# Kernel tuning notes

Measured on AMD Instinct MI355X. Metric: run time of the kernel, lower is better.

## Reference

```python
import jax, jax.numpy as jnp
import numpy as np
from jax import lax

B, C, H, W = 4, 512, 32, 32
HEADS, HC, GROUPS = 8, 64, 4
GC = C // GROUPS          # group channels = 128
GH = HEADS // GROUPS      # heads per group = 2
KK = 5                    # offset conv kernel (stage_idx=2)
OFFSET_RANGE_FACTOR = 2.0
LN_EPS = 1e-5


def conv1x1(x, w, b):
    # x: [B,Cin,H,W], w: [Cout,Cin], b: [Cout]
    return jnp.einsum('bchw,oc->bohw', x, w) + b[None, :, None, None]


def ref_points(h, w, n, dtype=jnp.float32):
    # torch linspace(0.5, h-0.5, h) normalized to (-1,1); stacked (y,x)
    ry = ((jnp.arange(h, dtype=dtype) + 0.5) / h) * 2.0 - 1.0
    rx = ((jnp.arange(w, dtype=dtype) + 0.5) / w) * 2.0 - 1.0
    ref = jnp.stack(jnp.meshgrid(ry, rx, indexing='ij'), axis=-1)  # [h,w,2]
    return jnp.broadcast_to(ref[None], (n, h, w, 2))


def grid_sample(img, grid):
    # F.grid_sample: bilinear, align_corners=True, padding_mode='zeros'
    # img: [N,C,Hs,Ws], grid: [N,*S,2] with grid[...,0]=x, grid[...,1]=y in [-1,1]
    N, Cc, Hs, Ws = img.shape
    gx = (grid[..., 0] + 1.0) * 0.5 * (Ws - 1)
    gy = (grid[..., 1] + 1.0) * 0.5 * (Hs - 1)
    x0 = jnp.floor(gx)
    y0 = jnp.floor(gy)
    wx1 = gx - x0
    wy1 = gy - y0
    imgf = img.reshape(N, Cc, Hs * Ws)

    def corner(ix, iy, wgt):
        valid = ((ix >= 0) & (ix <= Ws - 1) & (iy >= 0) & (iy <= Hs - 1)).astype(img.dtype)
        flat = (jnp.clip(iy, 0, Hs - 1) * Ws + jnp.clip(ix, 0, Ws - 1)).astype(jnp.int32)
        vals = jax.vmap(lambda im, f: im[:, f])(imgf, flat)  # [N,C,*S]
        return vals * (wgt * valid)[:, None]

    return (corner(x0, y0, (1 - wx1) * (1 - wy1))
            + corner(x0 + 1, y0, wx1 * (1 - wy1))
            + corner(x0, y0 + 1, (1 - wx1) * wy1)
            + corner(x0 + 1, y0 + 1, wx1 * wy1))


def setup_inputs() -> dict:
    key = jax.random.key(0)
    ks = jax.random.split(key, 10)

    def w(k, shape, s=0.02):
        return jax.random.normal(k, shape, jnp.float32) * s

    return {
        'x': jax.random.normal(ks[0], (B, C, H, W), jnp.float32),
        'w_q': w(ks[1], (C, C)), 'b_q': jnp.zeros((C,), jnp.float32),
        'w_k': w(ks[2], (C, C)), 'b_k': jnp.zeros((C,), jnp.float32),
        'w_v': w(ks[3], (C, C)), 'b_v': jnp.zeros((C,), jnp.float32),
        'w_o': w(ks[4], (C, C)), 'b_o': jnp.zeros((C,), jnp.float32),
        'dw_w': w(ks[5], (GC, 1, KK, KK), 0.05),  # depthwise offset conv
        'dw_b': jnp.zeros((GC,), jnp.float32),
        'ln_g': jnp.ones((GC,), jnp.float32),
        'ln_b': jnp.zeros((GC,), jnp.float32),
        'off_w': w(ks[6], (2, GC), 0.05),          # 1x1 conv -> 2 offset channels
        'rpe': w(ks[7], (HEADS, 2 * H - 1, 2 * W - 1), 0.01),
    }


def reference(x, w_q, b_q, w_k, b_k, w_v, b_v, w_o, b_o,
              dw_w, dw_b, ln_g, ln_b, off_w, rpe):
    q = conv1x1(x, w_q, b_q)
    # 'b (g c) h w -> (b g) c h w'
    q_off = q.reshape(B * GROUPS, GC, H, W)
    # depthwise conv kk=5, stride=1, pad=2
    off = lax.conv_general_dilated(q_off, dw_w, (1, 1),
                                   ((KK // 2, KK // 2), (KK // 2, KK // 2)),
                                   dimension_numbers=('NCHW', 'OIHW', 'NCHW'),
                                   feature_group_count=GC) + dw_b[None, :, None, None]
    # LayerNormProxy over channel dim
    mu = jnp.mean(off, axis=1, keepdims=True)
    var = jnp.mean((off - mu) ** 2, axis=1, keepdims=True)
    off = (off - mu) * lax.rsqrt(var + LN_EPS) * ln_g[None, :, None, None] + ln_b[None, :, None, None]
    off = jax.nn.gelu(off, approximate=False)
    off = jnp.einsum('bchw,oc->bohw', off, off_w)  # [B*G, 2, Hk, Wk] (y,x channels)
    Hk, Wk = off.shape[2], off.shape[3]
    nS = Hk * Wk
    off_range = jnp.array([1.0 / Hk, 1.0 / Wk], dtype=x.dtype).reshape(1, 2, 1, 1)
    off = jnp.tanh(off) * off_range * OFFSET_RANGE_FACTOR
    off = jnp.transpose(off, (0, 2, 3, 1))  # [B*G, Hk, Wk, 2]
    ref = ref_points(Hk, Wk, B * GROUPS, x.dtype)
    pos = off + ref  # offset_range_factor >= 0 branch
    # deformable sampling (grid takes (x,y))
    xs = grid_sample(x.reshape(B * GROUPS, GC, H, W), pos[..., ::-1])  # [B*G,GC,Hk,Wk]
    xs = xs.reshape(B, C, 1, nS)
    qf = q.reshape(B * HEADS, HC, H * W)
    k = conv1x1(xs, w_k, b_k).reshape(B * HEADS, HC, nS)
    v = conv1x1(xs, w_v, b_v).reshape(B * HEADS, HC, nS)
    attn = jnp.einsum('bcm,bcn->bmn', qf, k) * (HC ** -0.5)  # [B*Hd, HW, nS]
    # continuous relative-position bias via bilinear table lookup
    rpe_b = jnp.broadcast_to(rpe[None], (B,) + rpe.shape).reshape(
        B * GROUPS, GH, rpe.shape[1], rpe.shape[2])
    q_grid = ref_points(H, W, B * GROUPS, x.dtype)
    disp = (q_grid.reshape(B * GROUPS, H * W, 1, 2)
            - pos.reshape(B * GROUPS, 1, nS, 2)) * 0.5  # [B*G, HW, nS, 2]
    bias = grid_sample(rpe_b, disp[..., ::-1]).reshape(B * HEADS, H * W, nS)
    attn = jax.nn.softmax(attn + bias, axis=2)
    out = jnp.einsum('bmn,bcn->bcm', attn, v).reshape(B, C, H, W)
    y = conv1x1(out, w_o, b_o)
    return (y,
            pos.reshape(B, GROUPS, Hk, Wk, 2),
            ref.reshape(B, GROUPS, Hk, Wk, 2))
```

## Files before the change

### kernel.cpp

```cpp
#include <hip/hip_runtime.h>
#include <hip/hip_bf16.h>

typedef __hip_bfloat16 bf16;
typedef __attribute__((ext_vector_type(8))) short bf16x8;
typedef __attribute__((ext_vector_type(4))) float f32x4;

#define BDIM 4
#define CDIM 512
#define NHEADS 8
#define NGROUPS 4
#define GCH 128

__device__ __forceinline__ float bf2f(bf16 v) { return __bfloat162float(v); }
__device__ __forceinline__ float bfu2f(unsigned short u) {
  return __uint_as_float(((unsigned)u) << 16);
}
__device__ __forceinline__ unsigned short f2bu(float v) {
  return __hip_bfloat16_raw(__float2bfloat16(v)).x;
}
__device__ __forceinline__ unsigned pack2(float lo, float hi) {
  return (unsigned)f2bu(lo) | ((unsigned)f2bu(hi) << 16);
}

__global__ __launch_bounds__(256) void cvt_kernel(
    const float* __restrict__ x, const float* __restrict__ wq,
    const float* __restrict__ wk, const float* __restrict__ wv,
    const float* __restrict__ wo, unsigned short* __restrict__ x_bf,
    unsigned short* __restrict__ w_bf) {
  const int seg = blockIdx.y;
  const float* src;
  unsigned short* dst;
  int count;
  if (seg == 0) { src = x; dst = x_bf; count = 2097152; }
  else {
    src = (seg == 1 ? wq : seg == 2 ? wk : seg == 3 ? wv : wo);
    dst = w_bf + (seg - 1) * 262144;
    count = 262144;
  }
  const int i = (blockIdx.x * 256 + threadIdx.x) * 8;
  if (i >= count) return;
  const float4 a = *(const float4*)(src + i);
  const float4 b = *(const float4*)(src + i + 4);
  uint4 u;
  u.x = pack2(a.x, a.y);
  u.y = pack2(a.z, a.w);
  u.z = pack2(b.x, b.y);
  u.w = pack2(b.z, b.w);
  *(uint4*)(dst + i) = u;
}

template <typename OutT>
__global__ __launch_bounds__(256) void gemm_kernel(
    const unsigned short* __restrict__ Wb,
    const float* __restrict__ bias,
    const unsigned short* __restrict__ in,
    OutT* __restrict__ out) {
  __shared__ __align__(16) unsigned char smem[16384];
  unsigned char* a_lds = smem;
  unsigned char* b_lds = smem + 8192;
  const int b = blockIdx.z;
  const int o0 = blockIdx.y * 64;
  const int n0 = blockIdx.x * 64;
  const int t = threadIdx.x, l = t & 63, w = t >> 6;
  const int rg = l >> 4, cl = l & 15;
  const int o_base = (w >> 1) * 32, n_base = (w & 1) * 32;
  const unsigned short* inb = in + (size_t)b * 524288;
  const int ao = t >> 2;
  const int ac8 = (t & 3) * 8;
  const int kc2 = (t & 31) * 2;
  const int kn8 = (t >> 5) * 8;

  f32x4 acc[2][2] = {{{0.f,0.f,0.f,0.f},{0.f,0.f,0.f,0.f}},
                     {{0.f,0.f,0.f,0.f},{0.f,0.f,0.f,0.f}}};

  for (int k0 = 0; k0 < 512; k0 += 64) {
    {
      const uint4 wa = *(const uint4*)(Wb + (size_t)(o0 + ao) * 512 + k0 + ac8);
      const uint4 wb2 = *(const uint4*)(Wb + (size_t)(o0 + ao) * 512 + k0 + ac8 + 32);
      const unsigned swo = (unsigned)((ao & 7) << 4);
      *(uint4*)(a_lds + ao * 128 + ((2 * ac8) ^ swo)) = wa;
      *(uint4*)(a_lds + ao * 128 + ((2 * ac8 + 64) ^ swo)) = wb2;
    }
    {
      union { uint4 v; unsigned short hw[8]; } r0, r1;
      r0.v = *(const uint4*)(inb + (size_t)(k0 + kc2) * 1024 + n0 + kn8);
      r1.v = *(const uint4*)(inb + (size_t)(k0 + kc2 + 1) * 1024 + n0 + kn8);
#pragma unroll
      for (int i = 0; i < 8; i++) {
        const int n = kn8 + i;
        const unsigned v32 = (unsigned)r0.hw[i] | ((unsigned)r1.hw[i] << 16);
        *(unsigned*)(b_lds + n * 128 + ((2 * kc2) ^ ((n & 7) << 4))) = v32;
      }
    }
    __syncthreads();
#pragma unroll
    for (int kk = 0; kk < 2; kk++) {
      bf16x8 af[2], bfr[2];
#pragma unroll
      for (int m = 0; m < 2; m++) {
        const int o_loc = o_base + 16 * m + cl;
        af[m] = *(const bf16x8*)(a_lds + o_loc * 128 +
                                 ((64 * kk + 16 * rg) ^ ((o_loc & 7) << 4)));
      }
#pragma unroll
      for (int nn = 0; nn < 2; nn++) {
        const int n_loc = n_base + 16 * nn + cl;
        bfr[nn] = *(const bf16x8*)(b_lds + n_loc * 128 +
                                   ((64 * kk + 16 * rg) ^ ((n_loc & 7) << 4)));
      }
#pragma unroll
      for (int m = 0; m < 2; m++)
#pragma unroll
        for (int nn = 0; nn < 2; nn++)
          acc[m][nn] = __builtin_amdgcn_mfma_f32_16x16x32_bf16(af[m], bfr[nn],
                                                               acc[m][nn], 0, 0, 0);
    }
    __syncthreads();
  }

  float* o_st = (float*)smem;
#pragma unroll
  for (int m = 0; m < 2; m++)
#pragma unroll
    for (int nn = 0; nn < 2; nn++)
#pragma unroll
      for (int r = 0; r < 4; r++)
        o_st[(o_base + 16 * m + 4 * rg + r) * 64 + n_base + 16 * nn + cl] =
            acc[m][nn][r];
  __syncthreads();
  const int eo = t >> 4;
  const int en = (t & 15) * 4;
#pragma unroll
  for (int pass = 0; pass < 4; pass++) {
    const int o_loc = eo + pass * 16;
    const f32x4 v = *(const f32x4*)(o_st + o_loc * 64 + en);
    const float bv = bias[o0 + o_loc];
    if constexpr (sizeof(OutT) == 2) {
      ushort4 u;
      u.x = f2bu(v[0] + bv);
      u.y = f2bu(v[1] + bv);
      u.z = f2bu(v[2] + bv);
      u.w = f2bu(v[3] + bv);
      *(ushort4*)((bf16*)out + ((size_t)b * 512 + o0 + o_loc) * 1024 + n0 + en) = u;
    } else {
      float4 r = {v[0] + bv, v[1] + bv, v[2] + bv, v[3] + bv};
      *(float4*)((float*)out + ((size_t)b * 512 + o0 + o_loc) * 1024 + n0 + en) = r;
    }
  }
}

__global__ __launch_bounds__(512) void offset_kernel(
    const bf16* __restrict__ q, const float* __restrict__ dw_w,
    const float* __restrict__ dw_b, const float* __restrict__ ln_g,
    const float* __restrict__ ln_b, const float* __restrict__ off_w,
    float* __restrict__ pos, float* __restrict__ out_pos, float* __restrict__ out_ref) {
  __shared__ unsigned short q_s[5][36][128];
  __shared__ float red_a[4][2][2];
  __shared__ float red_p[4][2][2];
  const int bg = blockIdx.x;
  const int h = blockIdx.y;
  const int b = bg >> 2, g = bg & 3;
  const int t = threadIdx.x;

  for (int task = t; task < 640; task += 512) {
    const int ky = task >> 7, c = task & 127;
    const int y = h + ky - 2;
    if (y >= 0 && y < 32) {
      const unsigned short* qrow =
          (const unsigned short*)q + ((size_t)b * CDIM + g * GCH + c) * 1024 + y * 32;
      q_s[ky][0][c] = 0;
      q_s[ky][1][c] = 0;
#pragma unroll
      for (int x8 = 0; x8 < 4; x8++) {
        union { uint4 u; unsigned short s[8]; } vv;
        vv.u = *(const uint4*)(qrow + x8 * 8);
#pragma unroll
        for (int i = 0; i < 8; i++) q_s[ky][2 + x8 * 8 + i][c] = vv.s[i];
      }
      q_s[ky][34][c] = 0;
      q_s[ky][35][c] = 0;
    } else {
#pragma unroll
      for (int xi = 0; xi < 36; xi++) q_s[ky][xi][c] = 0;
    }
  }

  const int wslot = t >> 7;
  const int c = t & 127;
  const int half = c >> 6;
  const int lane = t & 63;
  float wgt[25];
#pragma unroll
  for (int i = 0; i < 25; i++) wgt[i] = dw_w[c * 25 + i];
  const float cbias = dw_b[c];
  const float gam = ln_g[c], bet = ln_b[c];
  const float ow0 = off_w[c], ow1 = off_w[GCH + c];
  __syncthreads();

  for (int j = 0; j < 8; j++) {
    const int w = wslot * 8 + j;
    float s = cbias;
#pragma unroll
    for (int ky = 0; ky < 5; ky++)
#pragma unroll
      for (int kx = 0; kx < 5; kx++)
        s += wgt[ky * 5 + kx] * bfu2f(q_s[ky][w + kx][c]);
    float ssum = s, ssq = s * s;
#pragma unroll
    for (int o = 1; o < 64; o <<= 1) {
      ssum += __shfl_xor(ssum, o);
      ssq += __shfl_xor(ssq, o);
    }
    if (lane == 0) { red_a[wslot][half][0] = ssum; red_a[wslot][half][1] = ssq; }
    __syncthreads();
    const float mu = (red_a[wslot][0][0] + red_a[wslot][1][0]) * (1.0f / 128.0f);
    const float var = (red_a[wslot][0][1] + red_a[wslot][1][1]) * (1.0f / 128.0f) - mu * mu;
    const float xn = (s - mu) * rsqrtf(var + 1e-5f) * gam + bet;
    const float ge = 0.5f * xn * (1.0f + erff(xn * 0.70710678118654752f));
    float p0 = ow0 * ge, p1 = ow1 * ge;
#pragma unroll
    for (int o = 1; o < 64; o <<= 1) {
      p0 += __shfl_xor(p0, o);
      p1 += __shfl_xor(p1, o);
    }
    if (lane == 0) { red_p[wslot][half][0] = p0; red_p[wslot][half][1] = p1; }
    __syncthreads();
    if (c == 0) {
      const float oy = tanhf(red_p[wslot][0][0] + red_p[wslot][1][0]) * 0.0625f;
      const float ox = tanhf(red_p[wslot][0][1] + red_p[wslot][1][1]) * 0.0625f;
      const float ry = ((float)h + 0.5f) * (2.0f / 32.0f) - 1.0f;
      const float rx = ((float)w + 0.5f) * (2.0f / 32.0f) - 1.0f;
      const float py = oy + ry, px = ox + rx;
      const size_t idx = (size_t)bg * 1024 + h * 32 + w;
      pos[idx * 2] = py;
      pos[idx * 2 + 1] = px;
      out_pos[idx * 2] = py;
      out_pos[idx * 2 + 1] = px;
      out_ref[idx * 2] = ry;
      out_ref[idx * 2 + 1] = rx;
    }
  }
}

__global__ __launch_bounds__(256) void sample_kernel(
    const float* __restrict__ x, const float* __restrict__ pos, bf16* __restrict__ xs) {
  const int bg = blockIdx.x, c = blockIdx.y;
  const int b = bg >> 2, g = bg & 3;
  __shared__ float plane[1024];
  const float* xp = x + ((size_t)b * CDIM + g * GCH + c) * 1024;
  for (int i = threadIdx.x; i < 1024; i += 256) plane[i] = xp[i];
  __syncthreads();
  for (int s = threadIdx.x; s < 1024; s += 256) {
    const float py = pos[((size_t)bg * 1024 + s) * 2];
    const float px = pos[((size_t)bg * 1024 + s) * 2 + 1];
    const float gx = (px + 1.0f) * 15.5f;
    const float gy = (py + 1.0f) * 15.5f;
    const float x0f = floorf(gx), y0f = floorf(gy);
    const float wx = gx - x0f, wy = gy - y0f;
    const int ix = (int)x0f, iy = (int)y0f;
    float r = 0.0f;
    const bool vx0 = (ix >= 0) & (ix <= 31), vx1 = (ix + 1 >= 0) & (ix + 1 <= 31);
    const bool vy0 = (iy >= 0) & (iy <= 31), vy1 = (iy + 1 >= 0) & (iy + 1 <= 31);
    if (vy0 && vx0) r += plane[iy * 32 + ix] * (1.0f - wx) * (1.0f - wy);
    if (vy0 && vx1) r += plane[iy * 32 + ix + 1] * wx * (1.0f - wy);
    if (vy1 && vx0) r += plane[(iy + 1) * 32 + ix] * (1.0f - wx) * wy;
    if (vy1 && vx1) r += plane[(iy + 1) * 32 + ix + 1] * wx * wy;
    xs[((size_t)bg * GCH + c) * 1024 + s] = __float2bfloat16(r);
  }
}

__global__ __launch_bounds__(512) void attn_kernel(
    const bf16* __restrict__ q, const bf16* __restrict__ kk,
    const bf16* __restrict__ vv, const float* __restrict__ pos,
    const float* __restrict__ rpe, bf16* __restrict__ ao) {
  __shared__ __align__(16) unsigned char smem[68384];
  float* rpe_f = (float*)(smem + 49152);
  float* m_x = (float*)(smem + 67360);
  float* s_x = (float*)(smem + 67872);

  const int bh = blockIdx.y;
  const int m0 = blockIdx.x * 64;
  const int b = bh >> 3, h = bh & 7;
  const int g = h >> 1;
  const int bg = b * 4 + g;
  const int t = threadIdx.x, l = t & 63, w = t >> 6;
  const int wq = w & 3, half = w >> 2;
  const int rg = l >> 4, cl = l & 15;
  const int t2 = t & 255;
  const size_t hbase = ((size_t)b * CDIM + h * 64) * 1024;
  const unsigned short* qu = (const unsigned short*)q;

  unsigned char* k_base = smem + half * 8192;
  unsigned char* v_base = smem + 16384 + half * 8192;
  unsigned char* p_base = smem + 32768 + half * 8192;
  float* pos_a = (float*)(smem + 66336) + half * 128;

  for (int i = t; i < 65 * 66; i += 512) {
    const int y = i / 66, x = i - y * 66;
    float v = 0.0f;
    if (y >= 1 && y <= 63 && x >= 1 && x <= 63)
      v = rpe[h * 3969 + (y - 1) * 63 + (x - 1)];
    rpe_f[i] = v;
  }

  const int qloc = 16 * wq + cl;
  const int qm = m0 + qloc;
  const float qy15 = 15.5f * (((float)(qm >> 5) + 0.5f) * (2.0f / 32.0f) - 1.0f);
  const float qx15 = 15.5f * (((float)(qm & 31) + 0.5f) * (2.0f / 32.0f) - 1.0f);

  bf16x8 bq[2];
#pragma unroll
  for (int kc = 0; kc < 2; kc++) {
    bf16x8 a;
#pragma unroll
    for (int j = 0; j < 8; j++)
      a[j] = (short)qu[hbase + (size_t)(32 * kc + 8 * rg + j) * 1024 + qm];
    bq[kc] = a;
  }

  float rmax = -1e30f, rsum = 0.0f;
  f32x4 oacc[4] = {{0.f,0.f,0.f,0.f},{0.f,0.f,0.f,0.f},
                   {0.f,0.f,0.f,0.f},{0.f,0.f,0.f,0.f}};

  const float* posb = pos + (size_t)bg * 2048;
  const unsigned swl = (unsigned)((cl & 7) << 4);
  const int kc2 = (t2 & 31) * 2;
  const int kn8 = (t2 >> 5) * 8;
  const int vc = t2 >> 2;
  const int vh = (t2 & 3) * 32;

  for (int tile = 0; tile < 8; tile++) {
    const int n0 = half * 512 + tile * 64;
    {
      union { uint4 v; unsigned short hw[8]; } r0, r1;
      r0.v = *(const uint4*)(kk + hbase + (size_t)kc2 * 1024 + n0 + kn8);
      r1.v = *(const uint4*)(kk + hbase + (size_t)(kc2 + 1) * 1024 + n0 + kn8);
#pragma unroll
      for (int i = 0; i < 8; i++) {
        const int n = kn8 + i;
        const unsigned v32 = (unsigned)r0.hw[i] | ((unsigned)r1.hw[i] << 16);
        *(unsigned*)(k_base + n * 128 + ((kc2 * 2) ^ ((n & 7) << 4))) = v32;
      }
      const uint4 s0 = *(const uint4*)(vv + hbase + (size_t)vc * 1024 + n0 + vh / 2);
      const uint4 s1 = *(const uint4*)(vv + hbase + (size_t)vc * 1024 + n0 + vh / 2 + 8);
      *(uint4*)(v_base + vc * 128 + (vh ^ ((vc & 7) << 4))) = s0;
      *(uint4*)(v_base + vc * 128 + ((vh + 16) ^ ((vc & 7) << 4))) = s1;
      if (t2 < 128) pos_a[t2] = 31.0f - 15.5f * posb[2 * n0 + t2];
    }
    __syncthreads();

    f32x4 sf[4];
#pragma unroll
    for (int tn = 0; tn < 4; tn++) {
      const int nrow = 16 * tn + cl;
      const bf16x8 a0 = *(const bf16x8*)(k_base + nrow * 128 + ((16 * rg) ^ swl));
      const bf16x8 a1 = *(const bf16x8*)(k_base + nrow * 128 + ((64 + 16 * rg) ^ swl));
      f32x4 z = {0.f, 0.f, 0.f, 0.f};
      z = __builtin_amdgcn_mfma_f32_16x16x32_bf16(a0, bq[0], z, 0, 0, 0);
      z = __builtin_amdgcn_mfma_f32_16x16x32_bf16(a1, bq[1], z, 0, 0, 0);
      sf[tn] = z;
    }

#pragma unroll
    for (int tn = 0; tn < 4; tn++)
#pragma unroll
      for (int r = 0; r < 4; r++) {
        const int key = 16 * tn + 4 * rg + r;
        const float gyc = qy15 + pos_a[2 * key];
        const float gxc = qx15 + pos_a[2 * key + 1];
        const float y0f = floorf(gyc), x0f = floorf(gxc);
        const float wy = gyc - y0f, wx = gxc - x0f;
        const int iy1 = (int)y0f + 1, ix1 = (int)x0f + 1;
        const float* tp = rpe_f + iy1 * 66 + ix1;
        const float t00 = tp[0], t01 = tp[1];
        const float t10 = tp[66], t11 = tp[67];
        const float r0v = t00 + (t01 - t00) * wx;
        const float r1v = t10 + (t11 - t10) * wx;
        const float bias = r0v + (r1v - r0v) * wy;
        sf[tn][r] = sf[tn][r] * 0.125f + bias;
      }

    float tmax = sf[0][0];
#pragma unroll
    for (int tn = 0; tn < 4; tn++)
#pragma unroll
      for (int r = 0; r < 4; r++) tmax = fmaxf(tmax, sf[tn][r]);
    tmax = fmaxf(tmax, __shfl_xor(tmax, 16));
    tmax = fmaxf(tmax, __shfl_xor(tmax, 32));
    const float nmax = fmaxf(rmax, tmax);
    const float corr = __expf(rmax - nmax);
    rmax = nmax;
    float lsum = 0.0f;
    unsigned pw[8];
#pragma unroll
    for (int tn = 0; tn < 4; tn++) {
      const float p0 = __expf(sf[tn][0] - nmax);
      const float p1 = __expf(sf[tn][1] - nmax);
      const float p2 = __expf(sf[tn][2] - nmax);
      const float p3 = __expf(sf[tn][3] - nmax);
      lsum += (p0 + p1) + (p2 + p3);
      pw[2 * tn] = pack2(p0, p1);
      pw[2 * tn + 1] = pack2(p2, p3);
    }
    lsum += __shfl_xor(lsum, 16);
    lsum += __shfl_xor(lsum, 32);
    rsum = rsum * corr + lsum;
#pragma unroll
    for (int tc = 0; tc < 4; tc++) {
      oacc[tc][0] *= corr; oacc[tc][1] *= corr;
      oacc[tc][2] *= corr; oacc[tc][3] *= corr;
    }

#pragma unroll
    for (int tn = 0; tn < 4; tn++) {
      *(unsigned*)(p_base + qloc * 128 + ((2 * (16 * tn + 4 * rg)) ^ swl)) = pw[2 * tn];
      *(unsigned*)(p_base + qloc * 128 + ((2 * (16 * tn + 4 * rg) + 4) ^ swl)) = pw[2 * tn + 1];
    }

#pragma unroll
    for (int kc = 0; kc < 2; kc++) {
      const bf16x8 pb = *(const bf16x8*)(p_base + qloc * 128 + ((2 * (32 * kc + 8 * rg)) ^ swl));
#pragma unroll
      for (int tc = 0; tc < 4; tc++) {
        const int crow = 16 * tc + cl;
        const bf16x8 av = *(const bf16x8*)(v_base + crow * 128 + ((2 * (32 * kc + 8 * rg)) ^ swl));
        oacc[tc] = __builtin_amdgcn_mfma_f32_16x16x32_bf16(av, pb, oacc[tc], 0, 0, 0);
      }
    }
    __syncthreads();
  }

  if (l < 16) {
    m_x[half * 64 + wq * 16 + cl] = rmax;
    s_x[half * 64 + wq * 16 + cl] = rsum;
  }
  __syncthreads();
  const float m0v = m_x[wq * 16 + cl], m1v = m_x[64 + wq * 16 + cl];
  const float s0v = s_x[wq * 16 + cl], s1v = s_x[64 + wq * 16 + cl];
  const float M = fmaxf(m0v, m1v);
  const float f0 = __expf(m0v - M), f1 = __expf(m1v - M);
  const float inv = 1.0f / (f0 * s0v + f1 * s1v);
  const float scale = (half == 0 ? f0 : f1) * inv;
  float* o_st = (float*)smem;
  if (half == 0) {
#pragma unroll
    for (int tc = 0; tc < 4; tc++)
#pragma unroll
      for (int r = 0; r < 4; r++)
        o_st[(16 * tc + 4 * rg + r) * 66 + qloc] = oacc[tc][r] * scale;
  }
  __syncthreads();
  if (half == 1) {
#pragma unroll
    for (int tc = 0; tc < 4; tc++)
#pragma unroll
      for (int r = 0; r < 4; r++)
        o_st[(16 * tc + 4 * rg + r) * 66 + qloc] += oacc[tc][r] * scale;
  }
  __syncthreads();
  {
    const int c = t >> 3, mq = (t & 7) * 8;
    unsigned u[4];
#pragma unroll
    for (int i = 0; i < 4; i++)
      u[i] = pack2(o_st[c * 66 + mq + 2 * i], o_st[c * 66 + mq + 2 * i + 1]);
    uint4 outv = {u[0], u[1], u[2], u[3]};
    *(uint4*)(ao + hbase + (size_t)c * 1024 + m0 + mq) = outv;
  }
}

extern "C" void kernel_launch(void* const* d_in, const int* in_sizes, int n_in,
                              void* d_out, int out_size, void* d_ws, size_t ws_size,
                              hipStream_t stream) {
  const float* x    = (const float*)d_in[0];
  const float* w_q  = (const float*)d_in[1];
  const float* b_q  = (const float*)d_in[2];
  const float* w_k  = (const float*)d_in[3];
  const float* b_k  = (const float*)d_in[4];
  const float* w_v  = (const float*)d_in[5];
  const float* b_v  = (const float*)d_in[6];
  const float* w_o  = (const float*)d_in[7];
  const float* b_o  = (const float*)d_in[8];
  const float* dw_w = (const float*)d_in[9];
  const float* dw_b = (const float*)d_in[10];
  const float* ln_g = (const float*)d_in[11];
  const float* ln_b = (const float*)d_in[12];
  const float* off_w= (const float*)d_in[13];
  const float* rpe  = (const float*)d_in[14];

  float* out_y   = (float*)d_out;
  float* out_pos = out_y + 2097152;
  float* out_ref = out_pos + 32768;

  float* pos_ws = (float*)d_ws;
  bf16*  q_ws   = (bf16*)(pos_ws + 32768);
  bf16*  xs_ws  = q_ws + 2097152;
  bf16*  k_ws   = xs_ws + 2097152;
  bf16*  v_ws   = k_ws + 2097152;
  bf16*  w_bf   = v_ws + 2097152;
  bf16*  x_bf   = k_ws;
  bf16*  ao_ws  = xs_ws;

  unsigned short* w_bfu = (unsigned short*)w_bf;

  cvt_kernel<<<dim3(1024, 5), 256, 0, stream>>>(x, w_q, w_k, w_v, w_o,
                                                (unsigned short*)x_bf, w_bfu);
  gemm_kernel<bf16><<<dim3(16, 8, 4), 256, 0, stream>>>(
      w_bfu, b_q, (const unsigned short*)x_bf, q_ws);
  offset_kernel<<<dim3(16, 32), 512, 0, stream>>>(q_ws, dw_w, dw_b, ln_g, ln_b, off_w,
                                                  pos_ws, out_pos, out_ref);
  sample_kernel<<<dim3(16, 128), 256, 0, stream>>>(x, pos_ws, xs_ws);
  gemm_kernel<bf16><<<dim3(16, 8, 4), 256, 0, stream>>>(
      w_bfu + 262144, b_k, (const unsigned short*)xs_ws, k_ws);
  gemm_kernel<bf16><<<dim3(16, 8, 4), 256, 0, stream>>>(
      w_bfu + 2 * 262144, b_v, (const unsigned short*)xs_ws, v_ws);
  attn_kernel<<<dim3(16, 32), 512, 0, stream>>>(q_ws, k_ws, v_ws, pos_ws, rpe, ao_ws);
  gemm_kernel<float><<<dim3(16, 8, 4), 256, 0, stream>>>(
      w_bfu + 3 * 262144, b_o, (const unsigned short*)ao_ws, out_y);
}
```

Baseline: 118.3 us.

## Fuse fp32-to-bf16 conversion into GEMMs, merge K/V GEMMs, shrink attention LDS

Removes the separate conversion kernel: the GEMM now loads fp32 weights (and fp32 x for the Q projection) and packs them to bf16 while staging into LDS. The K and V projections are merged into one launch that shares the staged xs tile across two weight matrices. The attention kernel reuses the K buffer for the P tile, adding a barrier, which cuts LDS from about 68KB to 52KB and may allow more resident blocks. The trade-off is doubled fp32 weight read traffic and conversion work repeated across blocks.

```diff
diff --git a/kernel.cpp b/kernel.cpp
--- a/kernel.cpp
+++ b/kernel.cpp
@@ -22,66 +22,69 @@
   return (unsigned)f2bu(lo) | ((unsigned)f2bu(hi) << 16);
 }
 
-__global__ __launch_bounds__(256) void cvt_kernel(
-    const float* __restrict__ x, const float* __restrict__ wq,
-    const float* __restrict__ wk, const float* __restrict__ wv,
-    const float* __restrict__ wo, unsigned short* __restrict__ x_bf,
-    unsigned short* __restrict__ w_bf) {
-  const int seg = blockIdx.y;
-  const float* src;
-  unsigned short* dst;
-  int count;
-  if (seg == 0) { src = x; dst = x_bf; count = 2097152; }
-  else {
-    src = (seg == 1 ? wq : seg == 2 ? wk : seg == 3 ? wv : wo);
-    dst = w_bf + (seg - 1) * 262144;
-    count = 262144;
-  }
-  const int i = (blockIdx.x * 256 + threadIdx.x) * 8;
-  if (i >= count) return;
-  const float4 a = *(const float4*)(src + i);
-  const float4 b = *(const float4*)(src + i + 4);
-  uint4 u;
-  u.x = pack2(a.x, a.y);
-  u.y = pack2(a.z, a.w);
-  u.z = pack2(b.x, b.y);
-  u.w = pack2(b.z, b.w);
-  *(uint4*)(dst + i) = u;
-}
-
-template <typename OutT>
+template <bool IN_F32, typename OutT, int NMAT>
 __global__ __launch_bounds__(256) void gemm_kernel(
-    const unsigned short* __restrict__ Wb,
-    const float* __restrict__ bias,
-    const unsigned short* __restrict__ in,
-    OutT* __restrict__ out) {
-  __shared__ __align__(16) unsigned char smem[16384];
-  unsigned char* a_lds = smem;
-  unsigned char* b_lds = smem + 8192;
+    const float* __restrict__ W0, const float* __restrict__ bias0,
+    const float* __restrict__ W1, const float* __restrict__ bias1,
+    const void* __restrict__ in,
+    OutT* __restrict__ out0, OutT* __restrict__ out1) {
+  __shared__ __align__(16) unsigned char smem[8192 * (NMAT + 1)];
+  unsigned char* b_lds = smem + 8192 * NMAT;
   const int b = blockIdx.z;
   const int o0 = blockIdx.y * 64;
   const int n0 = blockIdx.x * 64;
   const int t = threadIdx.x, l = t & 63, w = t >> 6;
   const int rg = l >> 4, cl = l & 15;
   const int o_base = (w >> 1) * 32, n_base = (w & 1) * 32;
-  const unsigned short* inb = in + (size_t)b * 524288;
   const int ao = t >> 2;
   const int ac8 = (t & 3) * 8;
   const int kc2 = (t & 31) * 2;
   const int kn8 = (t >> 5) * 8;
-
-  f32x4 acc[2][2] = {{{0.f,0.f,0.f,0.f},{0.f,0.f,0.f,0.f}},
-                     {{0.f,0.f,0.f,0.f},{0.f,0.f,0.f,0.f}}};
+  const unsigned swo = (unsigned)((ao & 7) << 4);
+  const float* Ws[2] = {W0, W1};
+  const float* Bs[2] = {bias0, bias1};
+  OutT* Os[2] = {out0, out1};
+
+  f32x4 acc[NMAT][2][2];
+#pragma unroll
+  for (int m = 0; m < NMAT; m++)
+#pragma unroll
+    for (int i = 0; i < 2; i++)
+#pragma unroll
+      for (int j = 0; j < 2; j++) acc[m][i][j] = {0.f, 0.f, 0.f, 0.f};
 
   for (int k0 = 0; k0 < 512; k0 += 64) {
-    {
-      const uint4 wa = *(const uint4*)(Wb + (size_t)(o0 + ao) * 512 + k0 + ac8);
-      const uint4 wb2 = *(const uint4*)(Wb + (size_t)(o0 + ao) * 512 + k0 + ac8 + 32);
-      const unsigned swo = (unsigned)((ao & 7) << 4);
-      *(uint4*)(a_lds + ao * 128 + ((2 * ac8) ^ swo)) = wa;
-      *(uint4*)(a_lds + ao * 128 + ((2 * ac8 + 64) ^ swo)) = wb2;
-    }
-    {
+#pragma unroll
+    for (int m = 0; m < NMAT; m++) {
+      const float* wr = Ws[m] + (size_t)(o0 + ao) * 512 + k0;
+      const float4 a0 = *(const float4*)(wr + ac8);
+      const float4 a1 = *(const float4*)(wr + ac8 + 4);
+      const float4 c0 = *(const float4*)(wr + ac8 + 32);
+      const float4 c1 = *(const float4*)(wr + ac8 + 36);
+      uint4 ua = {pack2(a0.x, a0.y), pack2(a0.z, a0.w),
+                  pack2(a1.x, a1.y), pack2(a1.z, a1.w)};
+      uint4 ub = {pack2(c0.x, c0.y), pack2(c0.z, c0.w),
+                  pack2(c1.x, c1.y), pack2(c1.z, c1.w)};
+      unsigned char* am = smem + 8192 * m;
+      *(uint4*)(am + ao * 128 + ((2 * ac8) ^ swo)) = ua;
+      *(uint4*)(am + ao * 128 + ((2 * ac8 + 64) ^ swo)) = ub;
+    }
+    if constexpr (IN_F32) {
+      const float* inb = (const float*)in + (size_t)b * 524288;
+      const float* p0 = inb + (size_t)(k0 + kc2) * 1024 + n0 + kn8;
+      union { float4 v[2]; float f[8]; } r0, r1;
+      r0.v[0] = *(const float4*)p0;
+      r0.v[1] = *(const float4*)(p0 + 4);
+      r1.v[0] = *(const float4*)(p0 + 1024);
+      r1.v[1] = *(const float4*)(p0 + 1028);
+#pragma unroll
+      for (int i = 0; i < 8; i++) {
+        const int n = kn8 + i;
+        *(unsigned*)(b_lds + n * 128 + ((2 * kc2) ^ ((n & 7) << 4))) =
+            pack2(r0.f[i], r1.f[i]);
+      }
+    } else {
+      const unsigned short* inb = (const unsigned short*)in + (size_t)b * 524288;
       union { uint4 v; unsigned short hw[8]; } r0, r1;
       r0.v = *(const uint4*)(inb + (size_t)(k0 + kc2) * 1024 + n0 + kn8);
       r1.v = *(const uint4*)(inb + (size_t)(k0 + kc2 + 1) * 1024 + n0 + kn8);
@@ -95,13 +98,7 @@
     __syncthreads();
 #pragma unroll
     for (int kk = 0; kk < 2; kk++) {
-      bf16x8 af[2], bfr[2];
-#pragma unroll
-      for (int m = 0; m < 2; m++) {
-        const int o_loc = o_base + 16 * m + cl;
-        af[m] = *(const bf16x8*)(a_lds + o_loc * 128 +
-                                 ((64 * kk + 16 * rg) ^ ((o_loc & 7) << 4)));
-      }
+      bf16x8 bfr[2];
 #pragma unroll
       for (int nn = 0; nn < 2; nn++) {
         const int n_loc = n_base + 16 * nn + cl;
@@ -109,42 +106,56 @@
                                    ((64 * kk + 16 * rg) ^ ((n_loc & 7) << 4)));
       }
 #pragma unroll
-      for (int m = 0; m < 2; m++)
-#pragma unroll
-        for (int nn = 0; nn < 2; nn++)
-          acc[m][nn] = __builtin_amdgcn_mfma_f32_16x16x32_bf16(af[m], bfr[nn],
-                                                               acc[m][nn], 0, 0, 0);
+      for (int m = 0; m < NMAT; m++) {
+        bf16x8 af[2];
+#pragma unroll
+        for (int mi = 0; mi < 2; mi++) {
+          const int o_loc = o_base + 16 * mi + cl;
+          af[mi] = *(const bf16x8*)(smem + 8192 * m + o_loc * 128 +
+                                    ((64 * kk + 16 * rg) ^ ((o_loc & 7) << 4)));
+        }
+#pragma unroll
+        for (int mi = 0; mi < 2; mi++)
+#pragma unroll
+          for (int nn = 0; nn < 2; nn++)
+            acc[m][mi][nn] = __builtin_amdgcn_mfma_f32_16x16x32_bf16(
+                af[mi], bfr[nn], acc[m][mi][nn], 0, 0, 0);
+      }
     }
     __syncthreads();
   }
 
   float* o_st = (float*)smem;
 #pragma unroll
-  for (int m = 0; m < 2; m++)
-#pragma unroll
-    for (int nn = 0; nn < 2; nn++)
-#pragma unroll
-      for (int r = 0; r < 4; r++)
-        o_st[(o_base + 16 * m + 4 * rg + r) * 64 + n_base + 16 * nn + cl] =
-            acc[m][nn][r];
-  __syncthreads();
-  const int eo = t >> 4;
-  const int en = (t & 15) * 4;
-#pragma unroll
-  for (int pass = 0; pass < 4; pass++) {
-    const int o_loc = eo + pass * 16;
-    const f32x4 v = *(const f32x4*)(o_st + o_loc * 64 + en);
-    const float bv = bias[o0 + o_loc];
-    if constexpr (sizeof(OutT) == 2) {
-      ushort4 u;
-      u.x = f2bu(v[0] + bv);
-      u.y = f2bu(v[1] + bv);
-      u.z = f2bu(v[2] + bv);
-      u.w = f2bu(v[3] + bv);
-      *(ushort4*)((bf16*)out + ((size_t)b * 512 + o0 + o_loc) * 1024 + n0 + en) = u;
-    } else {
-      float4 r = {v[0] + bv, v[1] + bv, v[2] + bv, v[3] + bv};
-      *(float4*)((float*)out + ((size_t)b * 512 + o0 + o_loc) * 1024 + n0 + en) = r;
+  for (int m = 0; m < NMAT; m++) {
+    __syncthreads();
+#pragma unroll
+    for (int mi = 0; mi < 2; mi++)
+#pragma unroll
+      for (int nn = 0; nn < 2; nn++)
+#pragma unroll
+        for (int r = 0; r < 4; r++)
+          o_st[(o_base + 16 * mi + 4 * rg + r) * 64 + n_base + 16 * nn + cl] =
+              acc[m][mi][nn][r];
+    __syncthreads();
+    const int eo = t >> 4;
+    const int en = (t & 15) * 4;
+#pragma unroll
+    for (int pass = 0; pass < 4; pass++) {
+      const int o_loc = eo + pass * 16;
+      const f32x4 v = *(const f32x4*)(o_st + o_loc * 64 + en);
+      const float bv = Bs[m][o0 + o_loc];
+      if constexpr (sizeof(OutT) == 2) {
+        ushort4 u;
+        u.x = f2bu(v[0] + bv);
+        u.y = f2bu(v[1] + bv);
+        u.z = f2bu(v[2] + bv);
+        u.w = f2bu(v[3] + bv);
+        *(ushort4*)((bf16*)Os[m] + ((size_t)b * 512 + o0 + o_loc) * 1024 + n0 + en) = u;
+      } else {
+        float4 r = {v[0] + bv, v[1] + bv, v[2] + bv, v[3] + bv};
+        *(float4*)((float*)Os[m] + ((size_t)b * 512 + o0 + o_loc) * 1024 + n0 + en) = r;
+      }
     }
   }
 }
@@ -273,10 +284,10 @@
     const bf16* __restrict__ q, const bf16* __restrict__ kk,
     const bf16* __restrict__ vv, const float* __restrict__ pos,
     const float* __restrict__ rpe, bf16* __restrict__ ao) {
-  __shared__ __align__(16) unsigned char smem[68384];
-  float* rpe_f = (float*)(smem + 49152);
-  float* m_x = (float*)(smem + 67360);
-  float* s_x = (float*)(smem + 67872);
+  __shared__ __align__(16) unsigned char smem[51976];
+  float* rpe_f = (float*)(smem + 32768);
+  float* m_x = (float*)(smem + 50952);
+  float* s_x = (float*)(smem + 51464);
 
   const int bh = blockIdx.y;
   const int m0 = blockIdx.x * 64;
@@ -292,8 +303,7 @@
 
   unsigned char* k_base = smem + half * 8192;
   unsigned char* v_base = smem + 16384 + half * 8192;
-  unsigned char* p_base = smem + 32768 + half * 8192;
-  float* pos_a = (float*)(smem + 66336) + half * 128;
+  float* pos_a = (float*)(smem + 49928) + half * 128;
 
   for (int i = t; i < 65 * 66; i += 512) {
     const int y = i / 66, x = i - y * 66;
@@ -411,15 +421,17 @@
       oacc[tc][2] *= corr; oacc[tc][3] *= corr;
     }
 
+    __syncthreads();
+
 #pragma unroll
     for (int tn = 0; tn < 4; tn++) {
-      *(unsigned*)(p_base + qloc * 128 + ((2 * (16 * tn + 4 * rg)) ^ swl)) = pw[2 * tn];
-      *(unsigned*)(p_base + qloc * 128 + ((2 * (16 * tn + 4 * rg) + 4) ^ swl)) = pw[2 * tn + 1];
+      *(unsigned*)(k_base + qloc * 128 + ((2 * (16 * tn + 4 * rg)) ^ swl)) = pw[2 * tn];
+      *(unsigned*)(k_base + qloc * 128 + ((2 * (16 * tn + 4 * rg) + 4) ^ swl)) = pw[2 * tn + 1];
     }
 
 #pragma unroll
     for (int kc = 0; kc < 2; kc++) {
-      const bf16x8 pb = *(const bf16x8*)(p_base + qloc * 128 + ((2 * (32 * kc + 8 * rg)) ^ swl));
+      const bf16x8 pb = *(const bf16x8*)(k_base + qloc * 128 + ((2 * (32 * kc + 8 * rg)) ^ swl));
 #pragma unroll
       for (int tc = 0; tc < 4; tc++) {
         const int crow = 16 * tc + cl;
@@ -497,24 +509,16 @@
   bf16*  xs_ws  = q_ws + 2097152;
   bf16*  k_ws   = xs_ws + 2097152;
   bf16*  v_ws   = k_ws + 2097152;
-  bf16*  w_bf   = v_ws + 2097152;
-  bf16*  x_bf   = k_ws;
   bf16*  ao_ws  = xs_ws;
 
-  unsigned short* w_bfu = (unsigned short*)w_bf;
-
-  cvt_kernel<<<dim3(1024, 5), 256, 0, stream>>>(x, w_q, w_k, w_v, w_o,
-                                                (unsigned short*)x_bf, w_bfu);
-  gemm_kernel<bf16><<<dim3(16, 8, 4), 256, 0, stream>>>(
-      w_bfu, b_q, (const unsigned short*)x_bf, q_ws);
+  gemm_kernel<true, bf16, 1><<<dim3(16, 8, 4), 256, 0, stream>>>(
+      w_q, b_q, nullptr, nullptr, x, q_ws, (bf16*)nullptr);
   offset_kernel<<<dim3(16, 32), 512, 0, stream>>>(q_ws, dw_w, dw_b, ln_g, ln_b, off_w,
                                                   pos_ws, out_pos, out_ref);
   sample_kernel<<<dim3(16, 128), 256, 0, stream>>>(x, pos_ws, xs_ws);
-  gemm_kernel<bf16><<<dim3(16, 8, 4), 256, 0, stream>>>(
-      w_bfu + 262144, b_k, (const unsigned short*)xs_ws, k_ws);
-  gemm_kernel<bf16><<<dim3(16, 8, 4), 256, 0, stream>>>(
-      w_bfu + 2 * 262144, b_v, (const unsigned short*)xs_ws, v_ws);
+  gemm_kernel<false, bf16, 2><<<dim3(16, 8, 4), 256, 0, stream>>>(
+      w_k, b_k, w_v, b_v, xs_ws, k_ws, v_ws);
   attn_kernel<<<dim3(16, 32), 512, 0, stream>>>(q_ws, k_ws, v_ws, pos_ws, rpe, ao_ws);
-  gemm_kernel<float><<<dim3(16, 8, 4), 256, 0, stream>>>(
-      w_bfu + 3 * 262144, b_o, (const unsigned short*)ao_ws, out_y);
-}
+  gemm_kernel<false, float, 1><<<dim3(16, 8, 4), 256, 0, stream>>>(
+      w_o, b_o, nullptr, nullptr, ao_ws, out_y, (float*)nullptr);
+}
```

Result: faster. 112.6 us (-4.8%).
